# Kernel tuning notes

Measured on AMD Instinct MI355X. Metric: run time of the kernel, lower is better.

## Reference

```python
import jax, jax.numpy as jnp
import numpy as np

# module hyperparameters (init kwargs)
D_MODEL = 1024
NUM_HEADS = 16
D_K = D_MODEL // NUM_HEADS
WINDOW_SIZE = 256
GLOBAL_TOKENS = 64
SEQ_LEN = 4096
BATCH = 1
NEG_INF = float('-inf')


def build_local_window_mask(seq_len, window_size, global_tokens):
    # 0 where attention is allowed, -inf where blocked
    i = jnp.arange(seq_len)[:, None]
    j = jnp.arange(seq_len)[None, :]
    allowed = (i < global_tokens) | (j < global_tokens) | (jnp.abs(i - j) <= window_size)
    return jnp.where(allowed, 0.0, NEG_INF).astype(jnp.float32)


def setup_inputs() -> dict:
    key = jax.random.key(0)
    ks = jax.random.split(key, 12)
    s = 1.0 / np.sqrt(D_MODEL)
    inp = {
        'q': jax.random.normal(ks[0], (BATCH, SEQ_LEN, D_MODEL), jnp.float32),
        'k': jax.random.normal(ks[1], (BATCH, SEQ_LEN, D_MODEL), jnp.float32),
        'v': jax.random.normal(ks[2], (BATCH, SEQ_LEN, D_MODEL), jnp.float32),
        # nn.Linear weights: shape (out, in), applied as x @ W.T + b
        'w_q': jax.random.normal(ks[3], (D_MODEL, D_MODEL), jnp.float32) * s,
        'b_q': jax.random.normal(ks[4], (D_MODEL,), jnp.float32) * s,
        'w_k': jax.random.normal(ks[5], (D_MODEL, D_MODEL), jnp.float32) * s,
        'b_k': jax.random.normal(ks[6], (D_MODEL,), jnp.float32) * s,
        'w_v': jax.random.normal(ks[7], (D_MODEL, D_MODEL), jnp.float32) * s,
        'b_v': jax.random.normal(ks[8], (D_MODEL,), jnp.float32) * s,
        'w_o': jax.random.normal(ks[9], (D_MODEL, D_MODEL), jnp.float32) * s,
        'b_o': jax.random.normal(ks[10], (D_MODEL,), jnp.float32) * s,
    }
    return inp


def reference(q, k, v, w_q, b_q, w_k, b_k, w_v, b_v, w_o, b_o):
    B, S, _ = q.shape
    scale = 1.0 / np.sqrt(D_K)

    def proj(x, w, b):  # (B,S,D) -> (B,H,S,Dk)
        y = x @ w.T + b
        return y.reshape(B, S, NUM_HEADS, D_K).transpose(0, 2, 1, 3)

    Q = proj(q, w_q, b_q)
    K = proj(k, w_k, b_k)
    V = proj(v, w_v, b_v)

    local_mask = build_local_window_mask(S, WINDOW_SIZE, GLOBAL_TOKENS)  # (S,S)
    scores = jnp.einsum('bhqd,bhkd->bhqk', Q, K) * scale + local_mask[None, None]
    attn = jax.nn.softmax(scores, axis=-1)
    out = jnp.einsum('bhqk,bhkd->bhqd', attn, V)  # (B,H,S,Dk)
    out = out.transpose(0, 2, 1, 3).reshape(B, S, D_MODEL)
    return out @ w_o.T + b_o
```

## Files before the change

kernel.cpp:

```cpp
#include <hip/hip_runtime.h>

#define S_LEN 4096
#define DMODEL 1024
#define NHEADS 16
#define DKH 64
#define WIN 256
#define GTOK 64
#define NSPLIT 8

typedef unsigned short u16t;
typedef __attribute__((ext_vector_type(8))) short short8;
typedef __attribute__((ext_vector_type(4))) float f32x4;

__device__ __forceinline__ u16t f2bf(float x) {
  union { float f; unsigned int u; } v; v.f = x;
  unsigned int r = v.u + 0x7FFFu + ((v.u >> 16) & 1u);
  return (u16t)(r >> 16);
}

__device__ __forceinline__ void gload_lds16(const u16t* g, u16t* l) {
  __builtin_amdgcn_global_load_lds(
      (const __attribute__((address_space(1))) void*)g,
      (__attribute__((address_space(3))) void*)l, 16, 0, 0);
}

__global__ void cvt4_kernel(const float* __restrict__ s0, const float* __restrict__ s1,
                            const float* __restrict__ s2, const float* __restrict__ s3,
                            u16t* __restrict__ d0, u16t* __restrict__ d1,
                            u16t* __restrict__ d2, u16t* __restrict__ d3) {
  size_t i = (size_t)blockIdx.x * 1024 + threadIdx.x * 4;
  int which = (int)(i >> 20);
  size_t local = i & ((1u << 20) - 1);
  const float* s = which == 0 ? s0 : which == 1 ? s1 : which == 2 ? s2 : s3;
  u16t* d = which == 0 ? d0 : which == 1 ? d1 : which == 2 ? d2 : d3;
  float4 f = *(const float4*)(s + local);
  unsigned int lo = (unsigned int)f2bf(f.x) | ((unsigned int)f2bf(f.y) << 16);
  unsigned int hi = (unsigned int)f2bf(f.z) | ((unsigned int)f2bf(f.w) << 16);
  *(uint2*)(d + local) = make_uint2(lo, hi);
}

__global__ void cvt3_kernel(const float* __restrict__ s0, const float* __restrict__ s1,
                            const float* __restrict__ s2,
                            u16t* __restrict__ d0, u16t* __restrict__ d1,
                            u16t* __restrict__ d2) {
  size_t i = (size_t)blockIdx.x * 1024 + threadIdx.x * 4;
  int which = (int)(i >> 22);
  size_t local = i & ((1u << 22) - 1);
  const float* s = which == 0 ? s0 : which == 1 ? s1 : s2;
  u16t* d = which == 0 ? d0 : which == 1 ? d1 : d2;
  float4 f = *(const float4*)(s + local);
  unsigned int lo = (unsigned int)f2bf(f.x) | ((unsigned int)f2bf(f.y) << 16);
  unsigned int hi = (unsigned int)f2bf(f.z) | ((unsigned int)f2bf(f.w) << 16);
  *(uint2*)(d + local) = make_uint2(lo, hi);
}

#define BN 128
#define GBK 64

template<int OUT_F32, int BMT, int BIAS_ROW>
__device__ __forceinline__
void gemm_body(const u16t* __restrict__ A, const u16t* __restrict__ B,
               const float* __restrict__ bias, void* __restrict__ Y,
               int N, int K, float alpha, int m0, int n0)
{
  constexpr int MF = BMT / 32;
  constexpr int CA_ISS = BMT * 2 / 64;

  __shared__ __align__(16) u16t sA[BMT * GBK];
  __shared__ __align__(16) u16t sB[BN * GBK];

  const int tid = threadIdx.x;
  const int lane = tid & 63;
  const int lr = lane & 15, lg = lane >> 4;
  const int w = tid >> 6;
  const int wm = (w >> 1) * (MF * 16), wn = (w & 1) * 64;

  f32x4 acc[MF][4] = {};
  const int nk = K / GBK;

  for (int kt = 0; kt < nk; ++kt) {
    if (kt) __syncthreads();
#pragma unroll
    for (int i = 0; i < CA_ISS; ++i) {
      int c0 = w * (BMT * 2) + i * 64;
      int c = c0 + lane;
      int row = c >> 3, g = (c & 7) ^ (row & 7);
      gload_lds16(A + (size_t)(m0 + row) * K + kt * GBK + g * 8, sA + (size_t)c0 * 8);
    }
#pragma unroll
    for (int i = 0; i < 4; ++i) {
      int c0 = w * 256 + i * 64;
      int c = c0 + lane;
      int row = c >> 3, g = (c & 7) ^ (row & 7);
      gload_lds16(B + (size_t)(n0 + row) * K + kt * GBK + g * 8, sB + (size_t)c0 * 8);
    }
    __syncthreads();

    short8 af[MF][2], bf[4][2];
#pragma unroll
    for (int mf = 0; mf < MF; ++mf)
#pragma unroll
      for (int kk = 0; kk < 2; ++kk) {
        int s = ((kk * 4 + lg) ^ (lr & 7));
        af[mf][kk] = *(const short8*)&sA[(wm + mf * 16 + lr) * GBK + s * 8];
      }
#pragma unroll
    for (int nf = 0; nf < 4; ++nf)
#pragma unroll
      for (int kk = 0; kk < 2; ++kk) {
        int s = ((kk * 4 + lg) ^ (lr & 7));
        bf[nf][kk] = *(const short8*)&sB[(wn + nf * 16 + lr) * GBK + s * 8];
      }
#pragma unroll
    for (int kk = 0; kk < 2; ++kk)
#pragma unroll
      for (int mf = 0; mf < MF; ++mf)
#pragma unroll
        for (int nf = 0; nf < 4; ++nf)
          acc[mf][nf] = __builtin_amdgcn_mfma_f32_16x16x32_bf16(af[mf][kk], bf[nf][kk], acc[mf][nf], 0, 0, 0);
  }

#pragma unroll
  for (int nf = 0; nf < 4; ++nf) {
    int col = n0 + wn + nf * 16 + lr;
    float bvc = BIAS_ROW ? 0.f : bias[col];
#pragma unroll
    for (int mf = 0; mf < MF; ++mf)
#pragma unroll
      for (int r = 0; r < 4; ++r) {
        int row = m0 + wm + mf * 16 + lg * 4 + r;
        float bv = BIAS_ROW ? bias[row] : bvc;
        float v = (acc[mf][nf][r] + bv) * alpha;
        if (OUT_F32) ((float*)Y)[(size_t)row * N + col] = v;
        else         ((u16t*)Y)[(size_t)row * N + col] = f2bf(v);
      }
  }
}

#define QSCALE 0.18033688011112042f
__global__ __launch_bounds__(256)
void gemm_qkv(const u16t* __restrict__ xq, const u16t* __restrict__ xk, const u16t* __restrict__ xv,
              const u16t* __restrict__ wq, const u16t* __restrict__ wk, const u16t* __restrict__ wv,
              const float* __restrict__ bq, const float* __restrict__ bk, const float* __restrict__ bv,
              u16t* __restrict__ Qp, u16t* __restrict__ Kp, u16t* __restrict__ Vt)
{
  int b = blockIdx.x;
  int wid = (b & 7) * 96 + (b >> 3);
  int z = wid >> 8;
  int rem = wid & 255;
  if (z == 0) {
    gemm_body<0, 128, 0>(xq, wq, bq, Qp, DMODEL, DMODEL, QSCALE, (rem >> 3) * 128, (rem & 7) * BN);
  } else if (z == 1) {
    gemm_body<0, 128, 0>(xk, wk, bk, Kp, DMODEL, DMODEL, 1.0f, (rem >> 3) * 128, (rem & 7) * BN);
  } else {
    gemm_body<0, 128, 1>(wv, xv, bv, Vt, S_LEN, DMODEL, 1.0f, (rem & 7) * 128, (rem >> 3) * BN);
  }
}

__global__ __launch_bounds__(256)
void gemm_o(const u16t* __restrict__ A, const u16t* __restrict__ B,
            const float* __restrict__ bias, float* __restrict__ Y)
{
  int b = blockIdx.x;
  int wid = (b & 7) * 64 + (b >> 3);
  int my = wid >> 3, mx = wid & 7;
  gemm_body<1, 64, 0>(A, B, bias, Y, DMODEL, DMODEL, 1.0f, my * 64, mx * BN);
}

#define KLDT 72

__global__ __launch_bounds__(256)
void attn_kernel(const u16t* __restrict__ Qp, const u16t* __restrict__ Kp,
                 const u16t* __restrict__ Vt, u16t* __restrict__ AO,
                 float* __restrict__ pacc, float* __restrict__ pml)
{
  __shared__ __align__(16) u16t sK[2][64 * 64];
  __shared__ __align__(16) u16t sV[2][64 * 64];
  __shared__ __align__(16) u16t sP[4][16 * KLDT];

  const int h = blockIdx.y;
  const int tid = threadIdx.x, w = tid >> 6, lane = tid & 63;
  const int lr = lane & 15, lg = lane >> 4;

  const bool windowed = (blockIdx.x < 63);
  const int qb = windowed ? (blockIdx.x + 1) : 0;
  const int split = windowed ? 0 : (blockIdx.x - 63);
  const int qw = qb * 64 + w * 16;

  short8 qf[2];
#pragma unroll
  for (int kk = 0; kk < 2; ++kk)
    qf[kk] = *(const short8*)(Qp + (size_t)(qw + lr) * DMODEL + h * DKH + kk * 32 + lg * 8);

  f32x4 acc[4] = {};
  float m_run = -1e30f, l_run = 0.f;

  int lo = 1, nkv;
  if (windowed) {
    lo = (qb - 4 < 1) ? 1 : qb - 4;
    int hi = (qb + 4 > 63) ? 63 : qb + 4;
    nkv = hi - lo + 2;
  } else {
    nkv = 64 / NSPLIT;
  }

#define KVB(idx) (windowed ? ((idx) == 0 ? 0 : lo + (idx) - 1) : (split * (64 / NSPLIT) + (idx)))

  auto stage = [&](int buf, int kvb) {
    int kv0 = kvb * 64;
#pragma unroll
    for (int j = 0; j < 2; ++j) {
      int c = tid + j * 256;
      int row = c >> 3, g = (c & 7) ^ (row & 7);
      gload_lds16(Kp + (size_t)(kv0 + row) * DMODEL + h * DKH + g * 8, &sK[buf][c * 8]);
    }
#pragma unroll
    for (int j = 0; j < 2; ++j) {
      int c = tid + j * 256;
      int row = c >> 3, g = (c & 7) ^ (row & 7);
      gload_lds16(Vt + (size_t)(h * DKH + row) * S_LEN + kv0 + g * 8, &sV[buf][c * 8]);
    }
  };

  stage(0, KVB(0));
  __syncthreads();

  for (int idx = 0; idx < nkv; ++idx) {
    const int buf = idx & 1;
    const int kvb = KVB(idx);
    const int kv0 = kvb * 64;

    if (idx + 1 < nkv) stage(buf ^ 1, KVB(idx + 1));

    f32x4 sacc[4] = {};
#pragma unroll
    for (int kk = 0; kk < 2; ++kk)
#pragma unroll
      for (int nf = 0; nf < 4; ++nf) {
        int s = ((kk * 4 + lg) ^ (lr & 7));
        short8 kf = *(const short8*)&sK[buf][(nf * 16 + lr) * 64 + s * 8];
        sacc[nf] = __builtin_amdgcn_mfma_f32_16x16x32_bf16(kf, qf[kk], sacc[nf], 0, 0, 0);
      }

    if (windowed && (kvb == qb + 4 || (kvb == qb - 4 && kvb > 0))) {
      int qg = qw + lr;
#pragma unroll
      for (int nf = 0; nf < 4; ++nf)
#pragma unroll
        for (int r = 0; r < 4; ++r) {
          int sg = kv0 + nf * 16 + lg * 4 + r;
          int diff = qg - sg; if (diff < 0) diff = -diff;
          if (diff > WIN) sacc[nf][r] = -1e30f;
        }
    }

    float rm = sacc[0][0];
#pragma unroll
    for (int nf = 0; nf < 4; ++nf)
#pragma unroll
      for (int r = 0; r < 4; ++r)
        rm = fmaxf(rm, sacc[nf][r]);
    rm = fmaxf(rm, __shfl_xor(rm, 16));
    rm = fmaxf(rm, __shfl_xor(rm, 32));

    if (!__all(rm <= m_run + 11.0f)) {
      float mnew = fmaxf(m_run, rm);
      float corr = exp2f(m_run - mnew);
      m_run = mnew;
      l_run *= corr;
      float cq[4];
#pragma unroll
      for (int r = 0; r < 4; ++r) cq[r] = __shfl(corr, lg * 4 + r);
#pragma unroll
      for (int nf = 0; nf < 4; ++nf)
#pragma unroll
        for (int r = 0; r < 4; ++r) acc[nf][r] *= cq[r];
    }

    float p[4][4];
    float rs = 0.f;
#pragma unroll
    for (int nf = 0; nf < 4; ++nf)
#pragma unroll
      for (int r = 0; r < 4; ++r) {
        float e = exp2f(sacc[nf][r] - m_run);
        p[nf][r] = e;
        rs += e;
      }
    rs += __shfl_xor(rs, 16);
    rs += __shfl_xor(rs, 32);
    l_run += rs;

#pragma unroll
    for (int nf = 0; nf < 4; ++nf) {
      uint2 w2;
      w2.x = (unsigned int)f2bf(p[nf][0]) | ((unsigned int)f2bf(p[nf][1]) << 16);
      w2.y = (unsigned int)f2bf(p[nf][2]) | ((unsigned int)f2bf(p[nf][3]) << 16);
      *(uint2*)&sP[w][lr * KLDT + nf * 16 + lg * 4] = w2;
    }

#pragma unroll
    for (int kk = 0; kk < 2; ++kk) {
      short8 pf = *(const short8*)&sP[w][lr * KLDT + kk * 32 + lg * 8];
#pragma unroll
      for (int nf = 0; nf < 4; ++nf) {
        int s = ((kk * 4 + lg) ^ (lr & 7));
        short8 vf = *(const short8*)&sV[buf][(nf * 16 + lr) * 64 + s * 8];
        acc[nf] = __builtin_amdgcn_mfma_f32_16x16x32_bf16(pf, vf, acc[nf], 0, 0, 0);
      }
    }

    if (idx + 1 < nkv) __syncthreads();
  }
#undef KVB

  if (windowed) {
    float lq[4];
#pragma unroll
    for (int r = 0; r < 4; ++r) lq[r] = __shfl(l_run, lg * 4 + r);
#pragma unroll
    for (int nf = 0; nf < 4; ++nf)
#pragma unroll
      for (int r = 0; r < 4; ++r) {
        float v = acc[nf][r] / lq[r];
        AO[(size_t)(qw + lg * 4 + r) * DMODEL + h * DKH + nf * 16 + lr] = f2bf(v);
      }
  } else {
    const int pbase = (h * NSPLIT + split) * 64;
#pragma unroll
    for (int nf = 0; nf < 4; ++nf)
#pragma unroll
      for (int r = 0; r < 4; ++r)
        pacc[(size_t)(pbase + w * 16 + lg * 4 + r) * 64 + nf * 16 + lr] = acc[nf][r];
    if (lane < 16) {
      int b = (pbase + w * 16 + lane) * 2;
      pml[b] = m_run;
      pml[b + 1] = l_run;
    }
  }
}

__global__ __launch_bounds__(256)
void merge_kernel(const float* __restrict__ pacc, const float* __restrict__ pml,
                  u16t* __restrict__ AO)
{
  const int h = blockIdx.x;
  const int tid = threadIdx.x;
  const int row = tid >> 2;
  const int d0 = (tid & 3) * 16;

  float M = -1e30f;
#pragma unroll
  for (int s = 0; s < NSPLIT; ++s)
    M = fmaxf(M, pml[((h * NSPLIT + s) * 64 + row) * 2]);

  float L = 0.f;
  float o[16];
#pragma unroll
  for (int e = 0; e < 16; ++e) o[e] = 0.f;

#pragma unroll
  for (int s = 0; s < NSPLIT; ++s) {
    int b = ((h * NSPLIT + s) * 64 + row) * 2;
    float sc = exp2f(pml[b] - M);
    L += pml[b + 1] * sc;
    const float4* a = (const float4*)(pacc + ((size_t)(h * NSPLIT + s) * 64 + row) * 64 + d0);
#pragma unroll
    for (int q4 = 0; q4 < 4; ++q4) {
      float4 av = a[q4];
      o[q4 * 4 + 0] += av.x * sc;
      o[q4 * 4 + 1] += av.y * sc;
      o[q4 * 4 + 2] += av.z * sc;
      o[q4 * 4 + 3] += av.w * sc;
    }
  }
  float inv = 1.f / L;
#pragma unroll
  for (int e = 0; e < 16; ++e)
    AO[(size_t)row * DMODEL + h * DKH + d0 + e] = f2bf(o[e] * inv);
}

extern "C" void kernel_launch(void* const* d_in, const int* in_sizes, int n_in,
                              void* d_out, int out_size, void* d_ws, size_t ws_size,
                              hipStream_t stream) {
  const float* q   = (const float*)d_in[0];
  const float* k   = (const float*)d_in[1];
  const float* v   = (const float*)d_in[2];
  const float* w_q = (const float*)d_in[3];
  const float* b_q = (const float*)d_in[4];
  const float* w_k = (const float*)d_in[5];
  const float* b_k = (const float*)d_in[6];
  const float* w_v = (const float*)d_in[7];
  const float* b_v = (const float*)d_in[8];
  const float* w_o = (const float*)d_in[9];
  const float* b_o = (const float*)d_in[10];

  u16t* ws = (u16t*)d_ws;
  const size_t SZX = (size_t)S_LEN * DMODEL;
  const size_t SZW = (size_t)DMODEL * DMODEL;
  u16t* xq  = ws;
  u16t* xk  = xq + SZX;
  u16t* xv  = xk + SZX;
  u16t* wb0 = xv + SZX;
  u16t* wb1 = wb0 + SZW;
  u16t* wb2 = wb1 + SZW;
  u16t* wb3 = wb2 + SZW;
  u16t* Qp  = wb3 + SZW;
  u16t* Kp  = Qp + SZX;
  u16t* Vt  = Kp + SZX;
  u16t* AO  = xk;
  float* pacc = (float*)xq;
  float* pml  = pacc + (size_t)NHEADS * NSPLIT * 64 * 64;

  dim3 blk(256);

  cvt4_kernel<<<(int)(4 * SZW / 1024), blk, 0, stream>>>(w_q, w_k, w_v, w_o, wb0, wb1, wb2, wb3);
  cvt3_kernel<<<(int)(3 * SZX / 1024), blk, 0, stream>>>(q, k, v, xq, xk, xv);

  gemm_qkv<<<768, blk, 0, stream>>>(xq, xk, xv, wb0, wb1, wb2, b_q, b_k, b_v, Qp, Kp, Vt);

  attn_kernel<<<dim3(63 + NSPLIT, NHEADS), blk, 0, stream>>>(Qp, Kp, Vt, AO, pacc, pml);
  merge_kernel<<<NHEADS, blk, 0, stream>>>(pacc, pml, AO);

  gemm_o<<<512, blk, 0, stream>>>(AO, wb3, b_o, (float*)d_out);
}
```

Baseline: 122.2 us.

## Merge conversion kernels, add MFMA priority hints, swizzle P tile, use packed bf16 cvt

Merges the two fp32-to-bf16 conversion launches into one kernel that covers weights and activations, saving a launch and its tail. Wraps the MFMA loops in the GEMM and attention kernels with s_setprio so waves issuing matrix ops get scheduler priority. In attention, the padded P scratch tile becomes an XOR-swizzled unpadded layout, P is packed with the hardware v_cvt_pk_bf16_f32 instruction, and the row-max reduction becomes a shallower tree. The packed convert may round differently from the manual round-to-nearest-even, and the priority hints may not help.

New measurement: 117.7 us. 1.04x faster.

```diff
diff --git a/kernel.cpp b/kernel.cpp
--- a/kernel.cpp
+++ b/kernel.cpp
@@ -18,36 +18,40 @@
   return (u16t)(r >> 16);
 }
 
+__device__ __forceinline__ unsigned int cvtpk(float lo, float hi) {
+  unsigned int r;
+  asm("v_cvt_pk_bf16_f32 %0, %1, %2" : "=v"(r) : "v"(lo), "v"(hi));
+  return r;
+}
+
 __device__ __forceinline__ void gload_lds16(const u16t* g, u16t* l) {
   __builtin_amdgcn_global_load_lds(
       (const __attribute__((address_space(1))) void*)g,
       (__attribute__((address_space(3))) void*)l, 16, 0, 0);
 }
 
-__global__ void cvt4_kernel(const float* __restrict__ s0, const float* __restrict__ s1,
-                            const float* __restrict__ s2, const float* __restrict__ s3,
-                            u16t* __restrict__ d0, u16t* __restrict__ d1,
-                            u16t* __restrict__ d2, u16t* __restrict__ d3) {
+__global__ void cvt_all(const float* __restrict__ s0, const float* __restrict__ s1,
+                        const float* __restrict__ s2, const float* __restrict__ s3,
+                        const float* __restrict__ s4, const float* __restrict__ s5,
+                        const float* __restrict__ s6,
+                        u16t* __restrict__ d0, u16t* __restrict__ d1,
+                        u16t* __restrict__ d2, u16t* __restrict__ d3,
+                        u16t* __restrict__ d4, u16t* __restrict__ d5,
+                        u16t* __restrict__ d6) {
   size_t i = (size_t)blockIdx.x * 1024 + threadIdx.x * 4;
-  int which = (int)(i >> 20);
-  size_t local = i & ((1u << 20) - 1);
-  const float* s = which == 0 ? s0 : which == 1 ? s1 : which == 2 ? s2 : s3;
-  u16t* d = which == 0 ? d0 : which == 1 ? d1 : which == 2 ? d2 : d3;
-  float4 f = *(const float4*)(s + local);
-  unsigned int lo = (unsigned int)f2bf(f.x) | ((unsigned int)f2bf(f.y) << 16);
-  unsigned int hi = (unsigned int)f2bf(f.z) | ((unsigned int)f2bf(f.w) << 16);
-  *(uint2*)(d + local) = make_uint2(lo, hi);
-}
-
-__global__ void cvt3_kernel(const float* __restrict__ s0, const float* __restrict__ s1,
-                            const float* __restrict__ s2,
-                            u16t* __restrict__ d0, u16t* __restrict__ d1,
-                            u16t* __restrict__ d2) {
-  size_t i = (size_t)blockIdx.x * 1024 + threadIdx.x * 4;
-  int which = (int)(i >> 22);
-  size_t local = i & ((1u << 22) - 1);
-  const float* s = which == 0 ? s0 : which == 1 ? s1 : s2;
-  u16t* d = which == 0 ? d0 : which == 1 ? d1 : d2;
+  const float* s; u16t* d; size_t local;
+  if (i < ((size_t)4 << 20)) {
+    int which = (int)(i >> 20);
+    local = i & ((1u << 20) - 1);
+    s = which == 0 ? s0 : which == 1 ? s1 : which == 2 ? s2 : s3;
+    d = which == 0 ? d0 : which == 1 ? d1 : which == 2 ? d2 : d3;
+  } else {
+    size_t j = i - ((size_t)4 << 20);
+    int which = (int)(j >> 22);
+    local = j & ((1u << 22) - 1);
+    s = which == 0 ? s4 : which == 1 ? s5 : s6;
+    d = which == 0 ? d4 : which == 1 ? d5 : d6;
+  }
   float4 f = *(const float4*)(s + local);
   unsigned int lo = (unsigned int)f2bf(f.x) | ((unsigned int)f2bf(f.y) << 16);
   unsigned int hi = (unsigned int)f2bf(f.z) | ((unsigned int)f2bf(f.w) << 16);
@@ -111,6 +115,7 @@
         int s = ((kk * 4 + lg) ^ (lr & 7));
         bf[nf][kk] = *(const short8*)&sB[(wn + nf * 16 + lr) * GBK + s * 8];
       }
+    __builtin_amdgcn_s_setprio(1);
 #pragma unroll
     for (int kk = 0; kk < 2; ++kk)
 #pragma unroll
@@ -118,6 +123,7 @@
 #pragma unroll
         for (int nf = 0; nf < 4; ++nf)
           acc[mf][nf] = __builtin_amdgcn_mfma_f32_16x16x32_bf16(af[mf][kk], bf[nf][kk], acc[mf][nf], 0, 0, 0);
+    __builtin_amdgcn_s_setprio(0);
   }
 
 #pragma unroll
@@ -167,8 +173,6 @@
   gemm_body<1, 64, 0>(A, B, bias, Y, DMODEL, DMODEL, 1.0f, my * 64, mx * BN);
 }
 
-#define KLDT 72
-
 __global__ __launch_bounds__(256)
 void attn_kernel(const u16t* __restrict__ Qp, const u16t* __restrict__ Kp,
                  const u16t* __restrict__ Vt, u16t* __restrict__ AO,
@@ -176,7 +180,7 @@
 {
   __shared__ __align__(16) u16t sK[2][64 * 64];
   __shared__ __align__(16) u16t sV[2][64 * 64];
-  __shared__ __align__(16) u16t sP[4][16 * KLDT];
+  __shared__ __align__(16) u16t sP[4][16 * 64];
 
   const int h = blockIdx.y;
   const int tid = threadIdx.x, w = tid >> 6, lane = tid & 63;
@@ -233,6 +237,7 @@
     if (idx + 1 < nkv) stage(buf ^ 1, KVB(idx + 1));
 
     f32x4 sacc[4] = {};
+    __builtin_amdgcn_s_setprio(1);
 #pragma unroll
     for (int kk = 0; kk < 2; ++kk)
 #pragma unroll
@@ -241,6 +246,7 @@
         short8 kf = *(const short8*)&sK[buf][(nf * 16 + lr) * 64 + s * 8];
         sacc[nf] = __builtin_amdgcn_mfma_f32_16x16x32_bf16(kf, qf[kk], sacc[nf], 0, 0, 0);
       }
+    __builtin_amdgcn_s_setprio(0);
 
     if (windowed && (kvb == qb + 4 || (kvb == qb - 4 && kvb > 0))) {
       int qg = qw + lr;
@@ -254,12 +260,12 @@
         }
     }
 
-    float rm = sacc[0][0];
-#pragma unroll
-    for (int nf = 0; nf < 4; ++nf)
-#pragma unroll
-      for (int r = 0; r < 4; ++r)
-        rm = fmaxf(rm, sacc[nf][r]);
+    float rm0 = fmaxf(fmaxf(sacc[0][0], sacc[0][1]), sacc[0][2]);
+    float rm1 = fmaxf(fmaxf(sacc[0][3], sacc[1][0]), sacc[1][1]);
+    float rm2 = fmaxf(fmaxf(sacc[1][2], sacc[1][3]), sacc[2][0]);
+    float rm3 = fmaxf(fmaxf(sacc[2][1], sacc[2][2]), sacc[2][3]);
+    float rm4 = fmaxf(fmaxf(sacc[3][0], sacc[3][1]), sacc[3][2]);
+    float rm = fmaxf(fmaxf(rm0, rm1), fmaxf(fmaxf(rm2, rm3), fmaxf(rm4, sacc[3][3])));
     rm = fmaxf(rm, __shfl_xor(rm, 16));
     rm = fmaxf(rm, __shfl_xor(rm, 32));
 
@@ -293,21 +299,23 @@
 
 #pragma unroll
     for (int nf = 0; nf < 4; ++nf) {
-      uint2 w2;
-      w2.x = (unsigned int)f2bf(p[nf][0]) | ((unsigned int)f2bf(p[nf][1]) << 16);
-      w2.y = (unsigned int)f2bf(p[nf][2]) | ((unsigned int)f2bf(p[nf][3]) << 16);
-      *(uint2*)&sP[w][lr * KLDT + nf * 16 + lg * 4] = w2;
+      unsigned int lo32 = cvtpk(p[nf][0], p[nf][1]);
+      unsigned int hi32 = cvtpk(p[nf][2], p[nf][3]);
+      int blk = (nf * 2 + (lg >> 1)) ^ (lr & 7);
+      *(uint2*)&sP[w][lr * 64 + blk * 8 + (lg & 1) * 4] = make_uint2(lo32, hi32);
     }
 
 #pragma unroll
     for (int kk = 0; kk < 2; ++kk) {
-      short8 pf = *(const short8*)&sP[w][lr * KLDT + kk * 32 + lg * 8];
+      short8 pf = *(const short8*)&sP[w][lr * 64 + (((kk * 4 + lg) ^ (lr & 7))) * 8];
+      __builtin_amdgcn_s_setprio(1);
 #pragma unroll
       for (int nf = 0; nf < 4; ++nf) {
         int s = ((kk * 4 + lg) ^ (lr & 7));
         short8 vf = *(const short8*)&sV[buf][(nf * 16 + lr) * 64 + s * 8];
         acc[nf] = __builtin_amdgcn_mfma_f32_16x16x32_bf16(pf, vf, acc[nf], 0, 0, 0);
       }
+      __builtin_amdgcn_s_setprio(0);
     }
 
     if (idx + 1 < nkv) __syncthreads();
@@ -414,8 +422,8 @@
 
   dim3 blk(256);
 
-  cvt4_kernel<<<(int)(4 * SZW / 1024), blk, 0, stream>>>(w_q, w_k, w_v, w_o, wb0, wb1, wb2, wb3);
-  cvt3_kernel<<<(int)(3 * SZX / 1024), blk, 0, stream>>>(q, k, v, xq, xk, xv);
+  cvt_all<<<(int)((4 * SZW + 3 * SZX) / 1024), blk, 0, stream>>>(
+      w_q, w_k, w_v, w_o, q, k, v, wb0, wb1, wb2, wb3, xq, xk, xv);
 
   gemm_qkv<<<768, blk, 0, stream>>>(xq, xk, xv, wb0, wb1, wb2, b_q, b_k, b_v, Qp, Kp, Vt);
 
```
